# Performance work log

Hardware: AMD Instinct MI355X
Metric: run time of the kernel (lower is better)

The kernel has to match this reference:

```python
import jax, jax.numpy as jnp
import numpy as np

D_MODEL = 1024
N_HEADS = 16
HEAD_DIM = 64
INNER = N_HEADS * HEAD_DIM
D_FF = 4096


def ln_novar(x, w, b):
    # mean-only 'layernorm' (no variance division), per original LayerNormNoVar
    u = jnp.mean(x, axis=-1, keepdims=True)
    return w * (x - u) + b


def setup_inputs() -> dict:
    key = jax.random.key(0)
    ks = jax.random.split(key, 12)
    s = lambda k, shape, scale: jax.random.normal(k, shape, dtype=jnp.float32) * scale
    inp = {
        "src": s(ks[0], (4, 2048, D_MODEL), 1.0),
        "pre_norm_w": jnp.ones((D_MODEL,), jnp.float32),
        "pre_norm_b": jnp.zeros((D_MODEL,), jnp.float32),
        "wq": s(ks[1], (D_MODEL, INNER), 0.02),
        "wk": s(ks[2], (D_MODEL, INNER), 0.02),
        "wv": s(ks[3], (D_MODEL, INNER), 0.02),
        "w_proj": s(ks[4], (INNER, D_MODEL), 0.02),
        "b_proj": jnp.zeros((D_MODEL,), jnp.float32),
        "norm1_w": jnp.ones((D_MODEL,), jnp.float32),
        "norm1_b": jnp.zeros((D_MODEL,), jnp.float32),
        "w1": s(ks[5], (D_MODEL, D_FF), 0.02),
        "b1": jnp.zeros((D_FF,), jnp.float32),
        "w2": s(ks[6], (D_FF, D_MODEL), 0.02),
        "b2": jnp.zeros((D_MODEL,), jnp.float32),
    }
    return inp


def reference(src, pre_norm_w, pre_norm_b, wq, wk, wv, w_proj, b_proj,
              norm1_w, norm1_b, w1, b1, w2, b2):
    B, N, _ = src.shape
    scale = HEAD_DIM ** -0.5
    x = ln_novar(src, pre_norm_w, pre_norm_b)
    q = (x @ wq).reshape(B, N, N_HEADS, HEAD_DIM)
    k = (x @ wk).reshape(B, N, N_HEADS, HEAD_DIM)
    v = (x @ wv).reshape(B, N, N_HEADS, HEAD_DIM)
    attn = jnp.einsum('bqhd,bkhd->bhqk', q, k) * scale
    attn = jax.nn.softmax(attn, axis=-1)
    o = jnp.einsum('bhqk,bkhd->bqhd', attn, v).reshape(B, N, INNER)
    o = o @ w_proj + b_proj
    src = src + o
    src = ln_novar(src, norm1_w, norm1_b)
    ff = jax.nn.relu(src @ w1 + b1) @ w2 + b2
    return src + ff
```

## Files before the change

### kernel.cpp

```cpp
#include <hip/hip_runtime.h>
#include <hip/hip_bf16.h>
#include <stdint.h>

typedef __hip_bfloat16 bf16;
typedef float f32x4 __attribute__((ext_vector_type(4)));
typedef float f32x16 __attribute__((ext_vector_type(16)));
typedef short v8s __attribute__((ext_vector_type(8)));
typedef __bf16 v8bf __attribute__((ext_vector_type(8)));
typedef unsigned int v4u __attribute__((ext_vector_type(4)));
typedef unsigned int u32;

static constexpr int MROWS = 8192;
static constexpr int DM    = 1024;
static constexpr int DFF   = 4096;
static constexpr int SEQ   = 2048;

__device__ __forceinline__ f32x4 mfma16(v8s a, v8s b, f32x4 c) {
  return __builtin_amdgcn_mfma_f32_16x16x32_bf16(
      __builtin_bit_cast(v8bf, a), __builtin_bit_cast(v8bf, b), c, 0, 0, 0);
}
__device__ __forceinline__ f32x16 mfma32(v8s a, v8s b, f32x16 c) {
  return __builtin_amdgcn_mfma_f32_32x32x16_bf16(
      __builtin_bit_cast(v8bf, a), __builtin_bit_cast(v8bf, b), c, 0, 0, 0);
}

__device__ __forceinline__ void gload_lds16(const void* g, void* l) {
  __builtin_amdgcn_global_load_lds(
      (const __attribute__((address_space(1))) void*)g,
      (__attribute__((address_space(3))) void*)l, 16, 0, 0);
}

__device__ __forceinline__ u32 cvtpk_bf16(float a, float b) {
  u32 r;
  asm("v_cvt_pk_bf16_f32 %0, %1, %2" : "=v"(r) : "v"(a), "v"(b));
  return r;
}
__device__ __forceinline__ void pl32swap(u32& x, u32& y) {
  asm volatile("v_permlane32_swap_b32 %0, %1" : "+v"(x), "+v"(y));
}
__device__ __forceinline__ float fast_exp2(float x) {
  float r;
  asm("v_exp_f32 %0, %1" : "=v"(r) : "v"(x));
  return r;
}

__global__ __launch_bounds__(256) void transpose_all(
    const float* __restrict__ wq, const float* __restrict__ wk,
    const float* __restrict__ wv, const float* __restrict__ wproj,
    const float* __restrict__ w1, const float* __restrict__ w2,
    bf16* __restrict__ WTqkv, bf16* __restrict__ WTprj,
    bf16* __restrict__ WT1, bf16* __restrict__ WT2) {
  __shared__ float tile[32][33];
  int t = blockIdx.x;
  const float* W;
  bf16* WT;
  int K, N, bx, by;
  if (t < 1024)      { W = wq;    WT = WTqkv;              K = N = 1024; bx = t & 31; by = t >> 5; }
  else if (t < 2048) { t -= 1024; W = wk;  WT = WTqkv + 1024 * 1024; K = N = 1024; bx = t & 31; by = t >> 5; }
  else if (t < 3072) { t -= 2048; W = wv;  WT = WTqkv + 2048 * 1024; K = N = 1024; bx = t & 31; by = t >> 5; }
  else if (t < 4096) { t -= 3072; W = wproj; WT = WTprj;   K = N = 1024; bx = t & 31; by = t >> 5; }
  else if (t < 8192) { t -= 4096; W = w1;  WT = WT1; K = 1024; N = 4096; bx = t & 127; by = t >> 7; }
  else               { t -= 8192; W = w2;  WT = WT2; K = 4096; N = 1024; bx = t & 31; by = t >> 5; }
  const int c0 = bx * 32, r0 = by * 32;
  const int tx = threadIdx.x & 31, ty = threadIdx.x >> 5;
  #pragma unroll
  for (int i = 0; i < 32; i += 8)
    tile[ty + i][tx] = W[(size_t)(r0 + ty + i) * N + c0 + tx];
  __syncthreads();
  #pragma unroll
  for (int i = 0; i < 32; i += 8)
    WT[(size_t)(c0 + ty + i) * K + r0 + tx] = __float2bfloat16(tile[tx][ty + i]);
}

__global__ __launch_bounds__(256) void ln_novar_kernel(
    const float* __restrict__ x, const float* __restrict__ w,
    const float* __restrict__ b, bf16* __restrict__ ob, float* __restrict__ of) {
  const int row = blockIdx.x;
  const int t = threadIdx.x;
  const float4 v = ((const float4*)(x + (size_t)row * DM))[t];
  float s = v.x + v.y + v.z + v.w;
  #pragma unroll
  for (int off = 32; off > 0; off >>= 1) s += __shfl_down(s, off, 64);
  __shared__ float wsum[4];
  if ((t & 63) == 0) wsum[t >> 6] = s;
  __syncthreads();
  const float u = (wsum[0] + wsum[1] + wsum[2] + wsum[3]) * (1.0f / DM);
  const float4 wv = ((const float4*)w)[t];
  const float4 bv = ((const float4*)b)[t];
  const float o0 = wv.x * (v.x - u) + bv.x;
  const float o1 = wv.y * (v.y - u) + bv.y;
  const float o2 = wv.z * (v.z - u) + bv.z;
  const float o3 = wv.w * (v.w - u) + bv.w;
  bf16* op = ob + (size_t)row * DM + t * 4;
  op[0] = __float2bfloat16(o0); op[1] = __float2bfloat16(o1);
  op[2] = __float2bfloat16(o2); op[3] = __float2bfloat16(o3);
  if (of) {
    float4 o4; o4.x = o0; o4.y = o1; o4.z = o2; o4.w = o3;
    ((float4*)(of + (size_t)row * DM))[t] = o4;
  }
}

template <int EPI>
__global__ __launch_bounds__(256) void gemm_bt(
    const bf16* __restrict__ A, const bf16* __restrict__ BT,
    bf16* __restrict__ Cb, float* __restrict__ Cf,
    const float* __restrict__ bias, const float* __restrict__ res,
    int M, int Nn, int K) {
  __shared__ __align__(16) bf16 As[128 * 64];
  __shared__ __align__(16) bf16 Bs[128 * 64];

  const int tid = threadIdx.x;
  const int lane = tid & 63;
  const int wave = tid >> 6;
  const int wr = wave >> 1, wc = wave & 1;

  const int nwg = gridDim.x;
  const int nbx = Nn / 128;
  int bid = (blockIdx.x & 7) * (nwg >> 3) + (blockIdx.x >> 3);
  const int GM = 4;
  const int grp = bid / (GM * nbx);
  const int rem = bid - grp * (GM * nbx);
  const int by = grp * GM + (rem & (GM - 1));
  const int bx = rem >> 2;
  const int tM = by * 128, tN = bx * 128;

  f32x4 acc[4][4] = {};
  const int nk = K / 64;

  for (int kt = 0; kt < nk; ++kt) {
    if (kt) __syncthreads();
    const int k0 = kt * 64;
    #pragma unroll
    for (int c = 0; c < 4; ++c) {
      const int slot = c * 256 + tid;
      const int row = slot >> 3, s = slot & 7;
      const int kk = ((s ^ (row & 7)) << 3);
      gload_lds16(A + (size_t)(tM + row) * K + k0 + kk, (void*)(As + slot * 8));
      gload_lds16(BT + (size_t)(tN + row) * K + k0 + kk, (void*)(Bs + slot * 8));
    }
    __syncthreads();

    #pragma unroll
    for (int kk = 0; kk < 2; ++kk) {
      const int kslot = kk * 4 + (lane >> 4);
      v8s af[4], bfr[4];
      #pragma unroll
      for (int m = 0; m < 4; ++m) {
        const int row = wr * 64 + m * 16 + (lane & 15);
        af[m] = *(const v8s*)(As + (row * 8 + (kslot ^ (row & 7))) * 8);
      }
      #pragma unroll
      for (int n = 0; n < 4; ++n) {
        const int row = wc * 64 + n * 16 + (lane & 15);
        bfr[n] = *(const v8s*)(Bs + (row * 8 + (kslot ^ (row & 7))) * 8);
      }
      __builtin_amdgcn_s_setprio(1);
      #pragma unroll
      for (int m = 0; m < 4; ++m)
        #pragma unroll
        for (int n = 0; n < 4; ++n)
          acc[m][n] = mfma16(af[m], bfr[n], acc[m][n]);
      __builtin_amdgcn_s_setprio(0);
    }
  }

  #pragma unroll
  for (int m = 0; m < 4; ++m) {
    #pragma unroll
    for (int n = 0; n < 4; ++n) {
      const int row0 = tM + wr * 64 + m * 16 + ((lane >> 4) << 2);
      const int col = tN + wc * 64 + n * 16 + (lane & 15);
      #pragma unroll
      for (int r = 0; r < 4; ++r) {
        const int row = row0 + r;
        float v = acc[m][n][r];
        if (EPI == 0) {
          Cb[(size_t)row * Nn + col] = __float2bfloat16(v);
        } else if (EPI == 1) {
          v += bias[col];
          v = fmaxf(v, 0.0f);
          Cb[(size_t)row * Nn + col] = __float2bfloat16(v);
        } else if (EPI == 2) {
          v += bias[col] + res[(size_t)row * Nn + col];
          Cf[(size_t)row * Nn + col] = v;
        } else {
          const int sec = tN >> 10;
          if (sec == 0) {
            Cb[(size_t)row * Nn + col] = __float2bfloat16(v);
          } else {
            const int b = row >> 11, nn2 = row & 2047;
            const int ktt = nn2 >> 6, key = nn2 & 63;
            if (sec == 1) {
              const int ck = col - 1024;
              const int h = ck >> 6, dc = (ck >> 3) & 7, e = ck & 7;
              bf16* krp = (bf16*)(void*)bias;
              krp[((size_t)((b * 16 + h) * 32 + ktt)) * 4096 + dc * 512 +
                  key * 8 + e] = __float2bfloat16(v);
            } else {
              const int cv = col - 2048;
              const int h = cv >> 6, d = cv & 63;
              const int kc = key >> 3, e2 = key & 7;
              bf16* vrp = (bf16*)(void*)res;
              vrp[((size_t)((b * 16 + h) * 32 + ktt)) * 4096 + kc * 512 +
                  d * 8 + e2] = __float2bfloat16(v);
            }
          }
        }
      }
    }
  }
}

#define PPV(i) ((i) < 16 ? s0[(i) & 15] : s1[(i) & 15])
__global__ __launch_bounds__(256, 4) void attn_kernel(
    const bf16* __restrict__ qkv, const bf16* __restrict__ krep,
    const bf16* __restrict__ vrep, bf16* __restrict__ ob) {
  const int qt = blockIdx.x & 15;
  const int bh = blockIdx.x >> 4;
  const int b = bh >> 4, h = bh & 15;
  const int tid = threadIdx.x;
  const int lane = tid & 63, wave = tid >> 6;
  const int c = lane & 31, hi = lane >> 5;
  const float CEXP = 0.180336880111120426f;

  __shared__ __align__(16) bf16 Ks[2][4096];
  __shared__ __align__(16) bf16 Vs[2][4096];

  const int qrow = qt * 128 + wave * 32 + c;
  const bf16* qp = qkv + (size_t)(b * SEQ + qrow) * 3072 + h * 64;
  v8s qf[4];
  #pragma unroll
  for (int ks = 0; ks < 4; ++ks)
    qf[ks] = *(const v8s*)(qp + ks * 16 + hi * 8);

  f32x16 o0 = {}, o1 = {};
  float lrow = 0.0f;

  const size_t tilebase = (size_t)(bh * 32) * 4096;
  #pragma unroll
  for (int j = 0; j < 2; ++j) {
    gload_lds16(krep + tilebase + (tid + j * 256) * 8, &Ks[0][(tid + j * 256) * 8]);
    gload_lds16(vrep + tilebase + (tid + j * 256) * 8, &Vs[0][(tid + j * 256) * 8]);
  }
  asm volatile("s_waitcnt vmcnt(0)" ::: "memory");
  __builtin_amdgcn_s_barrier();
  asm volatile("" ::: "memory");

  for (int kt = 0; kt < 32; ++kt) {
    const int cur = kt & 1;
    if (kt < 31) {
      const size_t nb = tilebase + (size_t)(kt + 1) * 4096;
      #pragma unroll
      for (int j = 0; j < 2; ++j) {
        gload_lds16(krep + nb + (tid + j * 256) * 8, &Ks[cur ^ 1][(tid + j * 256) * 8]);
        gload_lds16(vrep + nb + (tid + j * 256) * 8, &Vs[cur ^ 1][(tid + j * 256) * 8]);
      }
    }
    const bf16* KB = Ks[cur];
    const bf16* VB = Vs[cur];

    f32x16 s0 = {}, s1 = {};
    __builtin_amdgcn_s_setprio(1);
    #pragma unroll
    for (int ks = 0; ks < 4; ++ks) {
      const int ch = (2 * ks + hi) * 512;
      v8s a0 = *(const v8s*)(KB + ch + c * 8);
      v8s a1 = *(const v8s*)(KB + ch + (c + 32) * 8);
      s0 = mfma32(a0, qf[ks], s0);
      s1 = mfma32(a1, qf[ks], s1);
    }
    __builtin_amdgcn_s_setprio(0);

    float rs0 = 0.0f, rs1 = 0.0f;
    #pragma unroll
    for (int i = 0; i < 16; ++i) {
      s0[i] = fast_exp2(s0[i] * CEXP);
      s1[i] = fast_exp2(s1[i] * CEXP);
      rs0 += s0[i];
      rs1 += s1[i];
    }
    float rs = rs0 + rs1;
    rs += __shfl_xor(rs, 32, 64);
    lrow += rs;

    v8s pa[4];
    #pragma unroll
    for (int ks = 0; ks < 4; ++ks) {
      u32 x  = cvtpk_bf16(PPV(8 * ks + 0), PPV(8 * ks + 1));
      u32 y  = cvtpk_bf16(PPV(8 * ks + 4), PPV(8 * ks + 5));
      u32 x2 = cvtpk_bf16(PPV(8 * ks + 2), PPV(8 * ks + 3));
      u32 y2 = cvtpk_bf16(PPV(8 * ks + 6), PPV(8 * ks + 7));
      pl32swap(x, y);
      pl32swap(x2, y2);
      v4u w; w.x = x; w.y = x2; w.z = y; w.w = y2;
      pa[ks] = __builtin_bit_cast(v8s, w);
    }

    __builtin_amdgcn_s_setprio(1);
    #pragma unroll
    for (int ks = 0; ks < 4; ++ks) {
      const int ch = (2 * ks + hi) * 512;
      v8s b0 = *(const v8s*)(VB + ch + c * 8);
      v8s b1 = *(const v8s*)(VB + ch + (c + 32) * 8);
      o0 = mfma32(pa[ks], b0, o0);
      o1 = mfma32(pa[ks], b1, o1);
    }
    __builtin_amdgcn_s_setprio(0);

    asm volatile("s_waitcnt vmcnt(0)" ::: "memory");
    __builtin_amdgcn_s_barrier();
    asm volatile("" ::: "memory");
  }

  const float rl = 1.0f / lrow;
  const size_t orow0 = (size_t)(b * SEQ + qt * 128 + wave * 32);
  #pragma unroll
  for (int r = 0; r < 16; ++r) {
    const int q = (r & 3) + 8 * (r >> 2) + 4 * hi;
    const float rq = __shfl(rl, q, 64);
    bf16* op = ob + (orow0 + q) * DM + h * 64;
    op[c] = __float2bfloat16(o0[r] * rq);
    op[32 + c] = __float2bfloat16(o1[r] * rq);
  }
}

extern "C" void kernel_launch(void* const* d_in, const int* in_sizes, int n_in,
                              void* d_out, int out_size, void* d_ws,
                              size_t ws_size, hipStream_t stream) {
  const float* src   = (const float*)d_in[0];
  const float* pnw   = (const float*)d_in[1];
  const float* pnb   = (const float*)d_in[2];
  const float* wq    = (const float*)d_in[3];
  const float* wk    = (const float*)d_in[4];
  const float* wv    = (const float*)d_in[5];
  const float* wproj = (const float*)d_in[6];
  const float* bproj = (const float*)d_in[7];
  const float* n1w   = (const float*)d_in[8];
  const float* n1b   = (const float*)d_in[9];
  const float* w1    = (const float*)d_in[10];
  const float* b1    = (const float*)d_in[11];
  const float* w2    = (const float*)d_in[12];
  const float* b2    = (const float*)d_in[13];
  float* out = (float*)d_out;

  char* ws = (char*)d_ws;
  size_t off = 0;
  bf16* WTqkv = (bf16*)(ws + off); off += (size_t)3072 * 1024 * 2;
  bf16* WTprj = (bf16*)(ws + off); off += (size_t)1024 * 1024 * 2;
  bf16* WT1   = (bf16*)(ws + off); off += (size_t)4096 * 1024 * 2;
  bf16* WT2   = (bf16*)(ws + off); off += (size_t)1024 * 4096 * 2;
  bf16* xb    = (bf16*)(ws + off); off += (size_t)MROWS * DM * 2;
  bf16* qkvb  = (bf16*)(ws + off); off += (size_t)MROWS * 3072 * 2;
  bf16* obuf  = (bf16*)(ws + off); off += (size_t)MROWS * DM * 2;
  float* yf   = (float*)(ws + off); off += (size_t)MROWS * DM * 4;
  bf16* h1    = (bf16*)(ws + off); off += (size_t)MROWS * DFF * 2;
  bf16* krep = h1;
  bf16* vrep = h1 + (size_t)64 * SEQ * 64;

  const dim3 blk(256);

  transpose_all<<<dim3(12288), blk, 0, stream>>>(
      wq, wk, wv, wproj, w1, w2, WTqkv, WTprj, WT1, WT2);

  ln_novar_kernel<<<MROWS, blk, 0, stream>>>(src, pnw, pnb, xb, nullptr);

  gemm_bt<3><<<dim3((3072 / 128) * (MROWS / 128)), blk, 0, stream>>>(
      xb, WTqkv, qkvb, nullptr, (const float*)krep, (const float*)vrep,
      MROWS, 3072, 1024);

  attn_kernel<<<dim3(16 * 64), dim3(256), 0, stream>>>(qkvb, krep, vrep, obuf);

  gemm_bt<2><<<dim3((1024 / 128) * (MROWS / 128)), blk, 0, stream>>>(
      obuf, WTprj, nullptr, yf, bproj, src, MROWS, 1024, 1024);

  ln_novar_kernel<<<MROWS, blk, 0, stream>>>(yf, n1w, n1b, xb, out);

  gemm_bt<1><<<dim3((4096 / 128) * (MROWS / 128)), blk, 0, stream>>>(
      xb, WT1, h1, nullptr, b1, nullptr, MROWS, 4096, 1024);

  gemm_bt<2><<<dim3((1024 / 128) * (MROWS / 128)), blk, 0, stream>>>(
      h1, WT2, nullptr, out, b2, out, MROWS, 1024, 4096);
}
```

Before: 407.9 us.

## Store residual intermediates in bf16 and vectorize layernorm kernels

```diff
diff --git a/kernel.cpp b/kernel.cpp
--- a/kernel.cpp
+++ b/kernel.cpp
@@ -72,32 +72,76 @@
     WT[(size_t)(c0 + ty + i) * K + r0 + tx] = __float2bfloat16(tile[tx][ty + i]);
 }
 
-__global__ __launch_bounds__(256) void ln_novar_kernel(
+__global__ __launch_bounds__(256) void ln_f32(
     const float* __restrict__ x, const float* __restrict__ w,
-    const float* __restrict__ b, bf16* __restrict__ ob, float* __restrict__ of) {
-  const int row = blockIdx.x;
-  const int t = threadIdx.x;
-  const float4 v = ((const float4*)(x + (size_t)row * DM))[t];
-  float s = v.x + v.y + v.z + v.w;
-  #pragma unroll
-  for (int off = 32; off > 0; off >>= 1) s += __shfl_down(s, off, 64);
-  __shared__ float wsum[4];
-  if ((t & 63) == 0) wsum[t >> 6] = s;
-  __syncthreads();
-  const float u = (wsum[0] + wsum[1] + wsum[2] + wsum[3]) * (1.0f / DM);
-  const float4 wv = ((const float4*)w)[t];
-  const float4 bv = ((const float4*)b)[t];
-  const float o0 = wv.x * (v.x - u) + bv.x;
-  const float o1 = wv.y * (v.y - u) + bv.y;
-  const float o2 = wv.z * (v.z - u) + bv.z;
-  const float o3 = wv.w * (v.w - u) + bv.w;
-  bf16* op = ob + (size_t)row * DM + t * 4;
-  op[0] = __float2bfloat16(o0); op[1] = __float2bfloat16(o1);
-  op[2] = __float2bfloat16(o2); op[3] = __float2bfloat16(o3);
-  if (of) {
-    float4 o4; o4.x = o0; o4.y = o1; o4.z = o2; o4.w = o3;
-    ((float4*)(of + (size_t)row * DM))[t] = o4;
-  }
+    const float* __restrict__ b, bf16* __restrict__ ob) {
+  const int row = blockIdx.x * 4 + (threadIdx.x >> 6);
+  const int lane = threadIdx.x & 63;
+  const float* xp = x + (size_t)row * DM + lane * 16;
+  float v[16];
+  #pragma unroll
+  for (int i = 0; i < 4; ++i) {
+    float4 t = ((const float4*)xp)[i];
+    v[4 * i] = t.x; v[4 * i + 1] = t.y; v[4 * i + 2] = t.z; v[4 * i + 3] = t.w;
+  }
+  float s = 0.0f;
+  #pragma unroll
+  for (int i = 0; i < 16; ++i) s += v[i];
+  #pragma unroll
+  for (int off = 32; off; off >>= 1) s += __shfl_xor(s, off, 64);
+  const float u = s * (1.0f / DM);
+  const float* wp = w + lane * 16;
+  const float* bp = b + lane * 16;
+  u32 pk[8];
+  #pragma unroll
+  for (int i = 0; i < 8; ++i) {
+    float4 wv4 = ((const float4*)wp)[i >> 1];
+    float4 bv4 = ((const float4*)bp)[i >> 1];
+    const float w0 = (i & 1) ? wv4.z : wv4.x, w1 = (i & 1) ? wv4.w : wv4.y;
+    const float b0 = (i & 1) ? bv4.z : bv4.x, b1 = (i & 1) ? bv4.w : bv4.y;
+    pk[i] = cvtpk_bf16(w0 * (v[2 * i] - u) + b0, w1 * (v[2 * i + 1] - u) + b1);
+  }
+  uint4* op = (uint4*)(ob + (size_t)row * DM + lane * 16);
+  op[0] = make_uint4(pk[0], pk[1], pk[2], pk[3]);
+  op[1] = make_uint4(pk[4], pk[5], pk[6], pk[7]);
+}
+
+__global__ __launch_bounds__(256) void ln_bf16(
+    const bf16* __restrict__ x, const float* __restrict__ w,
+    const float* __restrict__ b, bf16* __restrict__ ob) {
+  const int row = blockIdx.x * 4 + (threadIdx.x >> 6);
+  const int lane = threadIdx.x & 63;
+  const bf16* xp = x + (size_t)row * DM + lane * 16;
+  float v[16];
+  #pragma unroll
+  for (int i = 0; i < 2; ++i) {
+    v8s t = ((const v8s*)xp)[i];
+    #pragma unroll
+    for (int j = 0; j < 8; ++j) {
+      u32 bits = ((u32)(unsigned short)t[j]) << 16;
+      v[8 * i + j] = __builtin_bit_cast(float, bits);
+    }
+  }
+  float s = 0.0f;
+  #pragma unroll
+  for (int i = 0; i < 16; ++i) s += v[i];
+  #pragma unroll
+  for (int off = 32; off; off >>= 1) s += __shfl_xor(s, off, 64);
+  const float u = s * (1.0f / DM);
+  const float* wp = w + lane * 16;
+  const float* bp = b + lane * 16;
+  u32 pk[8];
+  #pragma unroll
+  for (int i = 0; i < 8; ++i) {
+    float4 wv4 = ((const float4*)wp)[i >> 1];
+    float4 bv4 = ((const float4*)bp)[i >> 1];
+    const float w0 = (i & 1) ? wv4.z : wv4.x, w1 = (i & 1) ? wv4.w : wv4.y;
+    const float b0 = (i & 1) ? bv4.z : bv4.x, b1 = (i & 1) ? bv4.w : bv4.y;
+    pk[i] = cvtpk_bf16(w0 * (v[2 * i] - u) + b0, w1 * (v[2 * i + 1] - u) + b1);
+  }
+  uint4* op = (uint4*)(ob + (size_t)row * DM + lane * 16);
+  op[0] = make_uint4(pk[0], pk[1], pk[2], pk[3]);
+  op[1] = make_uint4(pk[4], pk[5], pk[6], pk[7]);
 }
 
 template <int EPI>
@@ -174,14 +218,16 @@
       for (int r = 0; r < 4; ++r) {
         const int row = row0 + r;
         float v = acc[m][n][r];
-        if (EPI == 0) {
-          Cb[(size_t)row * Nn + col] = __float2bfloat16(v);
-        } else if (EPI == 1) {
+        if (EPI == 1) {
           v += bias[col];
           v = fmaxf(v, 0.0f);
           Cb[(size_t)row * Nn + col] = __float2bfloat16(v);
-        } else if (EPI == 2) {
+        } else if (EPI == 4) {
           v += bias[col] + res[(size_t)row * Nn + col];
+          Cb[(size_t)row * Nn + col] = __float2bfloat16(v);
+        } else if (EPI == 5) {
+          const bf16* resb = (const bf16*)(const void*)res;
+          v += bias[col] + __bfloat162float(resb[(size_t)row * Nn + col]);
           Cf[(size_t)row * Nn + col] = v;
         } else {
           const int sec = tN >> 10;
@@ -352,7 +398,7 @@
   bf16* xb    = (bf16*)(ws + off); off += (size_t)MROWS * DM * 2;
   bf16* qkvb  = (bf16*)(ws + off); off += (size_t)MROWS * 3072 * 2;
   bf16* obuf  = (bf16*)(ws + off); off += (size_t)MROWS * DM * 2;
-  float* yf   = (float*)(ws + off); off += (size_t)MROWS * DM * 4;
+  bf16* yfb   = (bf16*)(ws + off); off += (size_t)MROWS * DM * 2;
   bf16* h1    = (bf16*)(ws + off); off += (size_t)MROWS * DFF * 2;
   bf16* krep = h1;
   bf16* vrep = h1 + (size_t)64 * SEQ * 64;
@@ -362,7 +408,7 @@
   transpose_all<<<dim3(12288), blk, 0, stream>>>(
       wq, wk, wv, wproj, w1, w2, WTqkv, WTprj, WT1, WT2);
 
-  ln_novar_kernel<<<MROWS, blk, 0, stream>>>(src, pnw, pnb, xb, nullptr);
+  ln_f32<<<dim3(MROWS / 4), blk, 0, stream>>>(src, pnw, pnb, xb);
 
   gemm_bt<3><<<dim3((3072 / 128) * (MROWS / 128)), blk, 0, stream>>>(
       xb, WTqkv, qkvb, nullptr, (const float*)krep, (const float*)vrep,
@@ -370,14 +416,14 @@
 
   attn_kernel<<<dim3(16 * 64), dim3(256), 0, stream>>>(qkvb, krep, vrep, obuf);
 
-  gemm_bt<2><<<dim3((1024 / 128) * (MROWS / 128)), blk, 0, stream>>>(
-      obuf, WTprj, nullptr, yf, bproj, src, MROWS, 1024, 1024);
-
-  ln_novar_kernel<<<MROWS, blk, 0, stream>>>(yf, n1w, n1b, xb, out);
+  gemm_bt<4><<<dim3((1024 / 128) * (MROWS / 128)), blk, 0, stream>>>(
+      obuf, WTprj, yfb, nullptr, bproj, src, MROWS, 1024, 1024);
+
+  ln_bf16<<<dim3(MROWS / 4), blk, 0, stream>>>(yfb, n1w, n1b, xb);
 
   gemm_bt<1><<<dim3((4096 / 128) * (MROWS / 128)), blk, 0, stream>>>(
       xb, WT1, h1, nullptr, b1, nullptr, MROWS, 4096, 1024);
 
-  gemm_bt<2><<<dim3((1024 / 128) * (MROWS / 128)), blk, 0, stream>>>(
-      h1, WT2, nullptr, out, b2, out, MROWS, 1024, 4096);
-}
+  gemm_bt<5><<<dim3((1024 / 128) * (MROWS / 128)), blk, 0, stream>>>(
+      h1, WT2, nullptr, out, b2, (const float*)xb, MROWS, 1024, 4096);
+}
```

Result: faster. 399.0 us (-2.2%).
